# Performance work log

Hardware: AMD Instinct MI355X
Metric: run time of the kernel (lower is better)

Reference implementation:

```python
import jax, jax.numpy as jnp
import numpy as np

H, D_NOPE, D_ROPE, D_V, L_KV, HID = 16, 128, 64, 128, 512, 2048
D_QK = D_NOPE + D_ROPE
THETA = 10000.0
EPS = 1e-6


def _rope(x, positions):
    # neox-style rotary over last dim (D_ROPE); x: [T, ..., D_ROPE]
    half = D_ROPE // 2
    inv_freq = 1.0 / (THETA ** (jnp.arange(half, dtype=jnp.float32) * 2.0 / D_ROPE))
    ang = positions.astype(jnp.float32)[:, None] * inv_freq[None, :]  # [T, half]
    shape = (x.shape[0],) + (1,) * (x.ndim - 2) + (half,)
    cos, sin = jnp.cos(ang).reshape(shape), jnp.sin(ang).reshape(shape)
    x1, x2 = x[..., :half], x[..., half:]
    return jnp.concatenate([x1 * cos - x2 * sin, x2 * cos + x1 * sin], axis=-1)


def _rmsnorm(x, w):
    var = jnp.mean(x * x, axis=-1, keepdims=True)
    return x * jax.lax.rsqrt(var + EPS) * w


def setup_inputs() -> dict:
    key = jax.random.key(0)
    ks = jax.random.split(key, 6)
    T = 4096
    s = lambda fan_in: 1.0 / np.sqrt(fan_in)
    return {
        "positions": jnp.arange(T, dtype=jnp.int32),
        "hidden_states": jax.random.normal(ks[0], (T, HID), jnp.float32),
        "Wq": jax.random.normal(ks[1], (HID, H * D_QK), jnp.float32) * s(HID),
        "Wkva": jax.random.normal(ks[2], (HID, L_KV + D_ROPE), jnp.float32) * s(HID),
        "kv_a_ln_w": jnp.ones((L_KV,), jnp.float32),
        "Wkvb": jax.random.normal(ks[3], (L_KV, H * (D_NOPE + D_V)), jnp.float32) * s(L_KV),
        "Wo": jax.random.normal(ks[4], (H * D_V, HID), jnp.float32) * s(H * D_V),
    }


def reference(positions, hidden_states, Wq, Wkva, kv_a_ln_w, Wkvb, Wo):
    T = hidden_states.shape[0]
    scaling = 1.0 / np.sqrt(D_QK)

    q = (hidden_states @ Wq).reshape(T, H, D_QK)
    q_nope, q_pe = q[..., :D_NOPE], q[..., D_NOPE:]

    latent = hidden_states @ Wkva                    # [T, L_KV + D_ROPE]
    kv_a = _rmsnorm(latent[:, :L_KV], kv_a_ln_w)     # [T, L_KV]
    k_pe = latent[:, L_KV:]                          # [T, D_ROPE] (shared across heads)

    kv = (kv_a @ Wkvb).reshape(T, H, D_NOPE + D_V)
    k_nope, v = kv[..., :D_NOPE], kv[..., D_NOPE:]

    q_pe = _rope(q_pe, positions)                    # [T, H, D_ROPE]
    k_pe = _rope(k_pe, positions)                    # [T, D_ROPE]

    q = jnp.concatenate([q_nope, q_pe], axis=-1)     # [T, H, D_QK]
    k = jnp.concatenate(
        [k_nope, jnp.broadcast_to(k_pe[:, None, :], (T, H, D_ROPE))], axis=-1)

    scores = jnp.einsum("thd,shd->hts", q, k) * scaling        # [H, T, T]
    causal = positions[:, None] >= positions[None, :]           # [T, T]
    scores = jnp.where(causal[None], scores, jnp.finfo(scores.dtype).min)
    attn = jax.nn.softmax(scores, axis=-1)
    out = jnp.einsum("hts,shd->thd", attn, v)                   # [T, H, D_V]
    return out.reshape(T, H * D_V) @ Wo                          # [T, HID]
```

## Files before the change

### kernel.cpp

```cpp
#include <hip/hip_runtime.h>
#include <hip/hip_bf16.h>

#define T_LEN 4096
#define HID_DIM 2048
#define NH 16
#define DNOPE 128
#define DROPE 64
#define DV 128
#define LKV 512
#define DQK 192

#define BN 64

typedef __attribute__((ext_vector_type(8))) __bf16 bf16x8;
typedef __attribute__((ext_vector_type(4))) float f32x4;
typedef __attribute__((ext_vector_type(4))) short s16x4;

__device__ __forceinline__ unsigned short f2b(float f) {
  unsigned u = __builtin_bit_cast(unsigned, f);
  unsigned r = (u + 0x7FFFu + ((u >> 16) & 1u)) >> 16;
  return (unsigned short)r;
}

#define GL2LDS16(gp, lp)                                                   \
// ... 139 lines not shown
            float sn, cs;
            __sincosf(p * inv, &sn, &cs);
            float x1 = acc[i][j][r] * scale, x2 = acc[i][j + 2][r] * scale;
            Qb[(size_t)t * DQK + DNOPE + idx]      = f2b(x1 * cs - x2 * sn);
            Qb[(size_t)t * DQK + DNOPE + 32 + idx] = f2b(x2 * cs + x1 * sn);
          }
        }
    }
  } else {
#pragma unroll
    for (int i = 0; i < 4; i++)
#pragma unroll
      for (int j = 0; j < 4; j++) {
        int col = n0 + wn + j * 16 + l16;
        if (col < LKV + DROPE)
#pragma unroll
          for (int r = 0; r < 4; r++)
            latentf[(size_t)(row0 + i * 16 + r) * (LKV + DROPE) + col] = acc[i][j][r];
      }
  }
}

__global__ __launch_bounds__(256) void k_gemm_wkvb(
    const unsigned short* __restrict__ A, const unsigned short* __restrict__ Bt,
    unsigned short* __restrict__ Kh, unsigned short* __restrict__ VT) {
  int m0 = blockIdx.y * 128, n0 = blockIdx.x * 128;
  GEMM_CORE(A, Bt, NH * 256, LKV, LKV, LKV)
#pragma unroll
  for (int i = 0; i < 4; i++)
#pragma unroll
    for (int j = 0; j < 4; j++) {
      int col = n0 + wn + j * 16 + l16;
      int h = col >> 8, c = col & 255;
#pragma unroll
      for (int r = 0; r < 4; r++) {
        int t = row0 + i * 16 + r;
        unsigned short v = f2b(acc[i][j][r]);
        if (c < 128) Kh[((size_t)h * T_LEN + t) * DQK + c] = v;
        else         VT[((size_t)(h * 128 + c - 128)) * T_LEN + t] = v;
      }
    }
}

__global__ __launch_bounds__(256) void k_prep_latent(
    const float* __restrict__ latent, const float* __restrict__ w,
    const int* __restrict__ pos,
    unsigned short* __restrict__ kva, unsigned short* __restrict__ Kh) {
  __shared__ float red[256];
  int t = blockIdx.x;
  const float* row = latent + (size_t)t * (LKV + DROPE);
  float ss = 0.f;
  for (int c = threadIdx.x; c < LKV; c += 256) { float v = row[c]; ss += v * v; }
  red[threadIdx.x] = ss;
  __syncthreads();
  for (int s = 128; s > 0; s >>= 1) {
    if (threadIdx.x < s) red[threadIdx.x] += red[threadIdx.x + s];
    __syncthreads();
  }
  float rs = rsqrtf(red[0] / (float)LKV + 1e-6f);
  for (int c = threadIdx.x; c < LKV; c += 256)
    kva[(size_t)t * LKV + c] = f2b(row[c] * rs * w[c]);
  if (threadIdx.x < DROPE) {
    int i = threadIdx.x;
    float p = (float)pos[t];
    float val;
    if (i < 32) {
      float x1 = row[LKV + i], x2 = row[LKV + i + 32];
      float inv = __expf(-(float)i * 0.2878231366242557f);
      float sn, cs; __sincosf(p * inv, &sn, &cs);
      val = x1 * cs - x2 * sn;
    } else {
      float x1 = row[LKV + i - 32], x2 = row[LKV + i];
      float inv = __expf(-(float)(i - 32) * 0.2878231366242557f);
      float sn, cs; __sincosf(p * inv, &sn, &cs);
      val = x2 * cs + x1 * sn;
    }
    unsigned short vb = f2b(val);
#pragma unroll
    for (int h = 0; h < NH; h++)
      Kh[((size_t)h * T_LEN + t) * DQK + DNOPE + i] = vb;
  }
}

__global__ __launch_bounds__(256, 4) void k_flash(
    const unsigned short* __restrict__ Qh, const unsigned short* __restrict__ Kh,
    const unsigned short* __restrict__ VT, unsigned short* __restrict__ attn) {
  int bx = blockIdx.x;
  int h = bx & 15;
  int idx = bx >> 4;
  int qb = (idx < 32) ? (63 - idx) : (idx - 32);
  int m0 = qb * 64;
  int ntiles = qb + 1;

  __shared__ unsigned short Ks[64 * 24 * 8];
  __shared__ unsigned short Vs[128 * 8 * 8];

  int tid = threadIdx.x, lane = tid & 63, w = tid >> 6;
  int quad = lane >> 4, l16 = lane & 15;
  int x = l16 & 7;

  const unsigned short* Qbase = Qh + (size_t)h * T_LEN * DQK;
  const unsigned short* Kbase = Kh + (size_t)h * T_LEN * DQK;
  const unsigned short* Vbase = VT + (size_t)h * DV * T_LEN;

  bf16x8 qf[6];
#pragma unroll
  for (int kk = 0; kk < 6; kk++)
    qf[kk] = *(const bf16x8*)(Qbase + (size_t)(m0 + w * 16 + l16) * DQK + kk * 32 + quad * 8);

  int koff[6], voff[4];
#pragma unroll
  for (int k = 0; k < 6; k++) {
    int c = tid + k * 256;
    int row = c / 24, sc = c - row * 24;
    int cg = (sc & 0x18) | ((sc ^ row) & 7);
    koff[k] = row * DQK + cg * 8;
  }
#pragma unroll
  for (int k = 0; k < 4; k++) {
    int c = tid + k * 256;
    int row = c >> 3, sc = c & 7;
    int cg = sc ^ (row & 7);
    voff[k] = row * T_LEN + cg * 8;
  }

  const unsigned short* kEp[4];
  const unsigned short* kOp[4];
  const unsigned short* vAp[4];
#pragma unroll
  for (int st = 0; st < 4; st++) {
    int rb = (st * 16 + l16) * 192;
    kEp[st] = Ks + rb + ((quad ^ x) * 8);
    kOp[st] = Ks + rb + ((((quad + 4) ^ x)) * 8);
    vAp[st] = Vs + l16 * 64 + (((st * 2 + (quad >> 1)) ^ x) * 8) + (quad & 1) * 4;
  }

  f32x4 Oacc[8] = {};
  float li = 0.f;

#if !HAVE_MFMA16
  int lA = l16 + ((quad & 1) << 5);
  int lB = lA + 16;
  bool lowq = (quad < 2);
  const unsigned short* vFp[2];
#pragma unroll
  for (int u = 0; u < 2; u++)
    vFp[u] = Vs + l16 * 64 + (((u * 4 + quad) ^ x) * 8);
#endif

  for (int j = 0; j < ntiles; j++) {
#pragma unroll
    for (int k = 0; k < 6; k++) GL2LDS16(Kbase + koff[k], &Ks[(tid + k * 256) * 8]);
#pragma unroll
    for (int k = 0; k < 4; k++) GL2LDS16(Vbase + voff[k], &Vs[(tid + k * 256) * 8]);
#pragma unroll
    for (int k = 0; k < 6; k++) koff[k] += BN * DQK;
#pragma unroll
    for (int k = 0; k < 4; k++) voff[k] += BN;
    __syncthreads();

    f32x4 Sc[4] = {};
#pragma unroll
    for (int kk = 0; kk < 6; kk++) {
#pragma unroll
      for (int st = 0; st < 4; st++) {
        const unsigned short* kp = ((kk & 1) ? kOp[st] : kEp[st]) + (kk >> 1) * 64;
        bf16x8 kb = *(const bf16x8*)kp;
        Sc[st] = __builtin_amdgcn_mfma_f32_16x16x32_bf16(kb, qf[kk], Sc[st], 0, 0, 0);
      }
    }

    if (j == qb) {
      int m = m0 + w * 16 + l16;
      int n0 = j * BN;
#pragma unroll
      for (int st = 0; st < 4; st++)
#pragma unroll
        for (int r = 0; r < 4; r++) {
          int s = n0 + st * 16 + quad * 4 + r;
          if (s > m) Sc[st][r] = -1e30f;
        }
    }

    unsigned p0[4], p1[4];
#pragma unroll
    for (int st = 0; st < 4; st++) {
      float e0 = __expf(Sc[st][0]);
      float e1 = __expf(Sc[st][1]);
      float e2 = __expf(Sc[st][2]);
      float e3 = __expf(Sc[st][3]);
      li += (e0 + e1) + (e2 + e3);
      p0[st] = __builtin_amdgcn_perm(__builtin_bit_cast(unsigned, e1),
                                     __builtin_bit_cast(unsigned, e0), 0x07060302u);
      p1[st] = __builtin_amdgcn_perm(__builtin_bit_cast(unsigned, e3),
                                     __builtin_bit_cast(unsigned, e2), 0x07060302u);
    }

#if HAVE_MFMA16
#pragma unroll
    for (int st = 0; st < 4; st++) {
      uint2 pbu; pbu.x = p0[st]; pbu.y = p1[st];
      s16x4 pb = __builtin_bit_cast(s16x4, pbu);
#pragma unroll
      for (int dt = 0; dt < 8; dt++) {
        s16x4 va = __builtin_bit_cast(s16x4, *(const uint2*)(vAp[st] + dt * 1024));
        Oacc[dt] = mfma16(va, pb, Oacc[dt]);
      }
    }
#else
#pragma unroll
    for (int u = 0; u < 2; u++) {
      int a0 = __shfl((int)p0[2 * u], lA, 64);
      int a1 = __shfl((int)p0[2 * u + 1], lA, 64);
      int b0 = __shfl((int)p1[2 * u], lA, 64);
      int b1 = __shfl((int)p1[2 * u + 1], lA, 64);
      int c0 = __shfl((int)p0[2 * u], lB, 64);
      int c1 = __shfl((int)p0[2 * u + 1], lB, 64);
      int d0 = __shfl((int)p1[2 * u], lB, 64);
      int d1 = __shfl((int)p1[2 * u + 1], lB, 64);
      int4 pk;
      pk.x = lowq ? a0 : a1;
      pk.y = lowq ? b0 : b1;
      pk.z = lowq ? c0 : c1;
      pk.w = lowq ? d0 : d1;
      bf16x8 pb = __builtin_bit_cast(bf16x8, pk);
#pragma unroll
      for (int dt = 0; dt < 8; dt++) {
        bf16x8 va = *(const bf16x8*)(vFp[u] + dt * 1024);
        Oacc[dt] = __builtin_amdgcn_mfma_f32_16x16x32_bf16(va, pb, Oacc[dt], 0, 0, 0);
      }
    }
#endif
    __syncthreads();
  }

  li += __shfl_xor(li, 16, 64);
  li += __shfl_xor(li, 32, 64);

  float inv = 1.f / li;
  int t = m0 + w * 16 + l16;
  unsigned short* dst = attn + (size_t)t * HID_DIM + h * DV + quad * 4;
#pragma unroll
  for (int dt = 0; dt < 8; dt++) {
    unsigned lo = (unsigned)f2b(Oacc[dt][0] * inv) |
                  ((unsigned)f2b(Oacc[dt][1] * inv) << 16);
    unsigned hi = (unsigned)f2b(Oacc[dt][2] * inv) |
                  ((unsigned)f2b(Oacc[dt][3] * inv) << 16);
    uint2 pk = {lo, hi};
    *(uint2*)(dst + dt * 16) = pk;
  }
}

extern "C" void kernel_launch(void* const* d_in, const int* in_sizes, int n_in,
                              void* d_out, int out_size, void* d_ws, size_t ws_size,
                              hipStream_t stream) {
  const int*   positions = (const int*)d_in[0];
  const float* hs   = (const float*)d_in[1];
  const float* Wq   = (const float*)d_in[2];
  const float* Wkva = (const float*)d_in[3];
  const float* lnw  = (const float*)d_in[4];
  const float* Wkvb = (const float*)d_in[5];
  const float* Wo   = (const float*)d_in[6];
  float* out = (float*)d_out;

  char* p = (char*)d_ws;
  size_t off = 0;
  auto alloc = [&](size_t bytes) {
    char* r = p + off;
    off = (off + bytes + 255) & ~(size_t)255;
    return r;
  };
  unsigned short* hsb     = (unsigned short*)alloc((size_t)T_LEN * HID_DIM * 2);
  unsigned short* WqT     = (unsigned short*)alloc((size_t)(NH * DQK) * HID_DIM * 2);
  unsigned short* WkvaT   = (unsigned short*)alloc((size_t)(LKV + DROPE) * HID_DIM * 2);
  unsigned short* WkvbT   = (unsigned short*)alloc((size_t)(NH * 256) * LKV * 2);
  unsigned short* WoT     = (unsigned short*)alloc((size_t)HID_DIM * HID_DIM * 2);
  unsigned short* Qh      = (unsigned short*)alloc((size_t)NH * T_LEN * DQK * 2);
  unsigned short* kva     = (unsigned short*)alloc((size_t)T_LEN * LKV * 2);
  unsigned short* Kh      = (unsigned short*)alloc((size_t)NH * T_LEN * DQK * 2);
  unsigned short* VT      = (unsigned short*)alloc((size_t)NH * DV * T_LEN * 2);
  unsigned short* attn    = (unsigned short*)alloc((size_t)T_LEN * HID_DIM * 2);
  float*          latentf = (float*)alloc((size_t)T_LEN * (LKV + DROPE) * 4);

  k_cvt<<<(T_LEN * HID_DIM + 255) / 256, 256, 0, stream>>>(hs, hsb, T_LEN * HID_DIM);
  k_transpose_all<<<13440, dim3(32, 8), 0, stream>>>(Wq, Wkva, Wkvb, Wo, WqT, WkvaT, WkvbT, WoT);

  k_gemm_proj<<<dim3(29, T_LEN / 128), 256, 0, stream>>>(hsb, WqT, WkvaT, positions, Qh, latentf);

  k_prep_latent<<<T_LEN, 256, 0, stream>>>(latentf, lnw, positions, kva, Kh);

  k_gemm_wkvb<<<dim3((NH * 256) / 128, T_LEN / 128), 256, 0, stream>>>(kva, WkvbT, Kh, VT);

  k_flash<<<dim3(1024), 256, 0, stream>>>(Qh, Kh, VT, attn);

  k_gemm128<<<dim3(HID_DIM / 128, T_LEN / 128), 256, 0, stream>>>(
      attn, WoT, out, HID_DIM, HID_DIM, HID_DIM, HID_DIM, HID_DIM);
}
```

Before: 502.8 us.

## Pair short and long query blocks per flash block with double-buffered K/V tiles

Each flash attention workgroup now handles two query blocks, a short one (pk) and its mirror long one (63-pk). Every staged K/V tile is shared by both, which halves K/V global-to-LDS traffic for the shared prefix and balances causal work across blocks. It also double-buffers K/V in LDS so the next tile loads while the current one computes. In exchange the grid shrinks to 512 blocks, register pressure roughly doubles (occupancy hint drops from 4 to 2) and LDS per block doubles.

```diff
diff --git a/kernel.cpp b/kernel.cpp
--- a/kernel.cpp
+++ b/kernel.cpp
@@ -245,18 +245,18 @@
   }
 }
 
-__global__ __launch_bounds__(256, 4) void k_flash(
+__global__ __launch_bounds__(256, 2) void k_flash(
     const unsigned short* __restrict__ Qh, const unsigned short* __restrict__ Kh,
     const unsigned short* __restrict__ VT, unsigned short* __restrict__ attn) {
   int bx = blockIdx.x;
   int h = bx & 15;
-  int idx = bx >> 4;
-  int qb = (idx < 32) ? (63 - idx) : (idx - 32);
-  int m0 = qb * 64;
-  int ntiles = qb + 1;
-
-  __shared__ unsigned short Ks[64 * 24 * 8];
-  __shared__ unsigned short Vs[128 * 8 * 8];
+  int pk = bx >> 4;
+  int qbS = pk, qbL = 63 - pk;
+  int m0S = qbS * 64, m0L = qbL * 64;
+  int NT = qbL + 1;
+
+  __shared__ unsigned short Ks[2 * 64 * 24 * 8];
+  __shared__ unsigned short Vs[2 * 128 * 8 * 8];
 
   int tid = threadIdx.x, lane = tid & 63, w = tid >> 6;
   int quad = lane >> 4, l16 = lane & 15;
@@ -266,10 +266,12 @@
   const unsigned short* Kbase = Kh + (size_t)h * T_LEN * DQK;
   const unsigned short* Vbase = VT + (size_t)h * DV * T_LEN;
 
-  bf16x8 qf[6];
-#pragma unroll
-  for (int kk = 0; kk < 6; kk++)
-    qf[kk] = *(const bf16x8*)(Qbase + (size_t)(m0 + w * 16 + l16) * DQK + kk * 32 + quad * 8);
+  bf16x8 qfL[6], qfS[6];
+#pragma unroll
+  for (int kk = 0; kk < 6; kk++) {
+    qfL[kk] = *(const bf16x8*)(Qbase + (size_t)(m0L + w * 16 + l16) * DQK + kk * 32 + quad * 8);
+    qfS[kk] = *(const bf16x8*)(Qbase + (size_t)(m0S + w * 16 + l16) * DQK + kk * 32 + quad * 8);
+  }
 
   int koff[6], voff[4];
 #pragma unroll
@@ -287,131 +289,198 @@
     voff[k] = row * T_LEN + cg * 8;
   }
 
-  const unsigned short* kEp[4];
-  const unsigned short* kOp[4];
-  const unsigned short* vAp[4];
+  int kEo[4], kOo[4], vAo[4];
 #pragma unroll
   for (int st = 0; st < 4; st++) {
     int rb = (st * 16 + l16) * 192;
-    kEp[st] = Ks + rb + ((quad ^ x) * 8);
-    kOp[st] = Ks + rb + ((((quad + 4) ^ x)) * 8);
-    vAp[st] = Vs + l16 * 64 + (((st * 2 + (quad >> 1)) ^ x) * 8) + (quad & 1) * 4;
-  }
-
-  f32x4 Oacc[8] = {};
-  float li = 0.f;
+    kEo[st] = rb + ((quad ^ x) * 8);
+    kOo[st] = rb + (((quad + 4) ^ x) * 8);
+    vAo[st] = l16 * 64 + (((st * 2 + (quad >> 1)) ^ x) * 8) + (quad & 1) * 4;
+  }
+
+  f32x4 OaccL[8] = {}, OaccS[8] = {};
+  float liL = 0.f, liS = 0.f;
+  int mL = m0L + w * 16 + l16;
+  int mS = m0S + w * 16 + l16;
 
 #if !HAVE_MFMA16
   int lA = l16 + ((quad & 1) << 5);
   int lB = lA + 16;
   bool lowq = (quad < 2);
-  const unsigned short* vFp[2];
+  int vFo[2];
 #pragma unroll
   for (int u = 0; u < 2; u++)
-    vFp[u] = Vs + l16 * 64 + (((u * 4 + quad) ^ x) * 8);
+    vFo[u] = l16 * 64 + (((u * 4 + quad) ^ x) * 8);
 #endif
 
-  for (int j = 0; j < ntiles; j++) {
-#pragma unroll
-    for (int k = 0; k < 6; k++) GL2LDS16(Kbase + koff[k], &Ks[(tid + k * 256) * 8]);
-#pragma unroll
-    for (int k = 0; k < 4; k++) GL2LDS16(Vbase + voff[k], &Vs[(tid + k * 256) * 8]);
-#pragma unroll
-    for (int k = 0; k < 6; k++) koff[k] += BN * DQK;
-#pragma unroll
-    for (int k = 0; k < 4; k++) voff[k] += BN;
+#define STAGE(buf)                                                                         \
+  do {                                                                                     \
+    unsigned short* ksd = Ks + (buf) * (64 * 24 * 8);                                      \
+    unsigned short* vsd = Vs + (buf) * (128 * 8 * 8);                                      \
+    _Pragma("unroll")                                                                      \
+    for (int k = 0; k < 6; k++) GL2LDS16(Kbase + koff[k], &ksd[(tid + k * 256) * 8]);      \
+    _Pragma("unroll")                                                                      \
+    for (int k = 0; k < 4; k++) GL2LDS16(Vbase + voff[k], &vsd[(tid + k * 256) * 8]);      \
+    _Pragma("unroll")                                                                      \
+    for (int k = 0; k < 6; k++) koff[k] += BN * DQK;                                       \
+    _Pragma("unroll")                                                                      \
+    for (int k = 0; k < 4; k++) voff[k] += BN;                                             \
+  } while (0)
+
+#if HAVE_MFMA16
+#define TILE_PV(DOSQ)                                                                      \
+    _Pragma("unroll")                                                                      \
+    for (int st = 0; st < 4; st++) {                                                       \
+      uint2 puL; puL.x = p0L[st]; puL.y = p1L[st];                                         \
+      s16x4 pbL = __builtin_bit_cast(s16x4, puL);                                          \
+      uint2 puS; puS.x = p0S[st]; puS.y = p1S[st];                                         \
+      s16x4 pbS = __builtin_bit_cast(s16x4, puS);                                          \
+      _Pragma("unroll")                                                                    \
+      for (int dt = 0; dt < 8; dt++) {                                                     \
+        s16x4 va = __builtin_bit_cast(s16x4, *(const uint2*)(VsB + vAo[st] + dt * 1024));  \
+        OaccL[dt] = mfma16(va, pbL, OaccL[dt]);                                            \
+        if (DOSQ) OaccS[dt] = mfma16(va, pbS, OaccS[dt]);                                  \
+      }                                                                                    \
+    }
+#else
+#define TILE_PV(DOSQ)                                                                      \
+    _Pragma("unroll")                                                                      \
+    for (int u = 0; u < 2; u++) {                                                          \
+      int a0 = __shfl((int)p0L[2 * u], lA, 64);                                            \
+      int a1 = __shfl((int)p0L[2 * u + 1], lA, 64);                                        \
+      int b0 = __shfl((int)p1L[2 * u], lA, 64);                                            \
+      int b1 = __shfl((int)p1L[2 * u + 1], lA, 64);                                        \
+      int c0 = __shfl((int)p0L[2 * u], lB, 64);                                            \
+      int c1 = __shfl((int)p0L[2 * u + 1], lB, 64);                                        \
+      int d0 = __shfl((int)p1L[2 * u], lB, 64);                                            \
+      int d1 = __shfl((int)p1L[2 * u + 1], lB, 64);                                        \
+      int4 pkLv;                                                                           \
+      pkLv.x = lowq ? a0 : a1; pkLv.y = lowq ? b0 : b1;                                    \
+      pkLv.z = lowq ? c0 : c1; pkLv.w = lowq ? d0 : d1;                                    \
+      bf16x8 pbL = __builtin_bit_cast(bf16x8, pkLv);                                       \
+      int4 pkSv = pkLv;                                                                    \
+      if (DOSQ) {                                                                          \
+        int sa0 = __shfl((int)p0S[2 * u], lA, 64);                                         \
+        int sa1 = __shfl((int)p0S[2 * u + 1], lA, 64);                                     \
+        int sb0 = __shfl((int)p1S[2 * u], lA, 64);                                         \
+        int sb1 = __shfl((int)p1S[2 * u + 1], lA, 64);                                     \
+        int sc0 = __shfl((int)p0S[2 * u], lB, 64);                                         \
+        int sc1 = __shfl((int)p0S[2 * u + 1], lB, 64);                                     \
+        int sd0 = __shfl((int)p1S[2 * u], lB, 64);                                         \
+        int sd1 = __shfl((int)p1S[2 * u + 1], lB, 64);                                     \
+        pkSv.x = lowq ? sa0 : sa1; pkSv.y = lowq ? sb0 : sb1;                              \
+        pkSv.z = lowq ? sc0 : sc1; pkSv.w = lowq ? sd0 : sd1;                              \
+      }                                                                                    \
+      bf16x8 pbS = __builtin_bit_cast(bf16x8, pkSv);                                       \
+      _Pragma("unroll")                                                                    \
+      for (int dt = 0; dt < 8; dt++) {                                                     \
+        bf16x8 va = *(const bf16x8*)(VsB + vFo[u] + dt * 1024);                            \
+        OaccL[dt] = __builtin_amdgcn_mfma_f32_16x16x32_bf16(va, pbL, OaccL[dt], 0, 0, 0);  \
+        if (DOSQ) OaccS[dt] = __builtin_amdgcn_mfma_f32_16x16x32_bf16(va, pbS, OaccS[dt], 0, 0, 0); \
+      }                                                                                    \
+    }
+#endif
+
+#define TILE_BODY(DOSQ)                                                                    \
+  {                                                                                        \
+    f32x4 ScL[4] = {}; f32x4 ScS[4] = {};                                                  \
+    _Pragma("unroll")                                                                      \
+    for (int kk = 0; kk < 6; kk++) {                                                       \
+      _Pragma("unroll")                                                                    \
+      for (int st = 0; st < 4; st++) {                                                     \
+        bf16x8 kb = *(const bf16x8*)(KsB + ((kk & 1) ? kOo[st] : kEo[st]) + (kk >> 1) * 64); \
+        ScL[st] = __builtin_amdgcn_mfma_f32_16x16x32_bf16(kb, qfL[kk], ScL[st], 0, 0, 0);  \
+        if (DOSQ) ScS[st] = __builtin_amdgcn_mfma_f32_16x16x32_bf16(kb, qfS[kk], ScS[st], 0, 0, 0); \
+      }                                                                                    \
+    }                                                                                      \
+    if (j == qbL) {                                                                        \
+      _Pragma("unroll")                                                                    \
+      for (int st = 0; st < 4; st++)                                                       \
+        _Pragma("unroll")                                                                  \
+        for (int r = 0; r < 4; r++) {                                                      \
+          int s = n0 + st * 16 + quad * 4 + r;                                             \
+          if (s > mL) ScL[st][r] = -1e30f;                                                 \
+        }                                                                                  \
+    }                                                                                      \
+    if (DOSQ && j == qbS) {                                                                \
+      _Pragma("unroll")                                                                    \
+      for (int st = 0; st < 4; st++)                                                       \
+        _Pragma("unroll")                                                                  \
+        for (int r = 0; r < 4; r++) {                                                      \
+          int s = n0 + st * 16 + quad * 4 + r;                                             \
+          if (s > mS) ScS[st][r] = -1e30f;                                                 \
+        }                                                                                  \
+    }                                                                                      \
+    unsigned p0L[4], p1L[4], p0S[4], p1S[4];                                               \
+    _Pragma("unroll")                                                                      \
+    for (int st = 0; st < 4; st++) {                                                       \
+      float e0 = __expf(ScL[st][0]);                                                       \
+      float e1 = __expf(ScL[st][1]);                                                       \
+      float e2 = __expf(ScL[st][2]);                                                       \
+      float e3 = __expf(ScL[st][3]);                                                       \
+      liL += (e0 + e1) + (e2 + e3);                                                        \
+      p0L[st] = __builtin_amdgcn_perm(__builtin_bit_cast(unsigned, e1),                    \
+                                      __builtin_bit_cast(unsigned, e0), 0x07060302u);      \
+      p1L[st] = __builtin_amdgcn_perm(__builtin_bit_cast(unsigned, e3),                    \
+                                      __builtin_bit_cast(unsigned, e2), 0x07060302u);      \
+      if (DOSQ) {                                                                          \
+        float f0 = __expf(ScS[st][0]);                                                     \
+        float f1 = __expf(ScS[st][1]);                                                     \
+        float f2 = __expf(ScS[st][2]);                                                     \
+        float f3 = __expf(ScS[st][3]);                                                     \
+        liS += (f0 + f1) + (f2 + f3);                                                      \
+        p0S[st] = __builtin_amdgcn_perm(__builtin_bit_cast(unsigned, f1),                  \
+                                        __builtin_bit_cast(unsigned, f0), 0x07060302u);    \
+        p1S[st] = __builtin_amdgcn_perm(__builtin_bit_cast(unsigned, f3),                  \
+                                        __builtin_bit_cast(unsigned, f2), 0x07060302u);    \
+      } else { p0S[st] = 0; p1S[st] = 0; }                                                 \
+    }                                                                                      \
+    TILE_PV(DOSQ)                                                                          \
+  }
+
+  STAGE(0);
+  __syncthreads();
+
+  for (int j = 0; j < NT; ++j) {
+    if (j + 1 < NT) STAGE((j + 1) & 1);
+    const unsigned short* KsB = Ks + (j & 1) * (64 * 24 * 8);
+    const unsigned short* VsB = Vs + (j & 1) * (128 * 8 * 8);
+    int n0 = j * BN;
+    if (j <= pk) {
+      TILE_BODY(1)
+    } else {
+      TILE_BODY(0)
+    }
     __syncthreads();
-
-    f32x4 Sc[4] = {};
-#pragma unroll
-    for (int kk = 0; kk < 6; kk++) {
-#pragma unroll
-      for (int st = 0; st < 4; st++) {
-        const unsigned short* kp = ((kk & 1) ? kOp[st] : kEp[st]) + (kk >> 1) * 64;
-        bf16x8 kb = *(const bf16x8*)kp;
-        Sc[st] = __builtin_amdgcn_mfma_f32_16x16x32_bf16(kb, qf[kk], Sc[st], 0, 0, 0);
-      }
-    }
-
-    if (j == qb) {
-      int m = m0 + w * 16 + l16;
-      int n0 = j * BN;
-#pragma unroll
-      for (int st = 0; st < 4; st++)
-#pragma unroll
-        for (int r = 0; r < 4; r++) {
-          int s = n0 + st * 16 + quad * 4 + r;
-          if (s > m) Sc[st][r] = -1e30f;
-        }
-    }
-
-    unsigned p0[4], p1[4];
-#pragma unroll
-    for (int st = 0; st < 4; st++) {
-      float e0 = __expf(Sc[st][0]);
-      float e1 = __expf(Sc[st][1]);
-      float e2 = __expf(Sc[st][2]);
-      float e3 = __expf(Sc[st][3]);
-      li += (e0 + e1) + (e2 + e3);
-      p0[st] = __builtin_amdgcn_perm(__builtin_bit_cast(unsigned, e1),
-                                     __builtin_bit_cast(unsigned, e0), 0x07060302u);
-      p1[st] = __builtin_amdgcn_perm(__builtin_bit_cast(unsigned, e3),
-                                     __builtin_bit_cast(unsigned, e2), 0x07060302u);
-    }
-
-#if HAVE_MFMA16
-#pragma unroll
-    for (int st = 0; st < 4; st++) {
-      uint2 pbu; pbu.x = p0[st]; pbu.y = p1[st];
-      s16x4 pb = __builtin_bit_cast(s16x4, pbu);
-#pragma unroll
-      for (int dt = 0; dt < 8; dt++) {
-        s16x4 va = __builtin_bit_cast(s16x4, *(const uint2*)(vAp[st] + dt * 1024));
-        Oacc[dt] = mfma16(va, pb, Oacc[dt]);
-      }
-    }
-#else
-#pragma unroll
-    for (int u = 0; u < 2; u++) {
-      int a0 = __shfl((int)p0[2 * u], lA, 64);
-      int a1 = __shfl((int)p0[2 * u + 1], lA, 64);
-      int b0 = __shfl((int)p1[2 * u], lA, 64);
-      int b1 = __shfl((int)p1[2 * u + 1], lA, 64);
-      int c0 = __shfl((int)p0[2 * u], lB, 64);
-      int c1 = __shfl((int)p0[2 * u + 1], lB, 64);
-      int d0 = __shfl((int)p1[2 * u], lB, 64);
-      int d1 = __shfl((int)p1[2 * u + 1], lB, 64);
-      int4 pk;
-      pk.x = lowq ? a0 : a1;
-      pk.y = lowq ? b0 : b1;
-      pk.z = lowq ? c0 : c1;
-      pk.w = lowq ? d0 : d1;
-      bf16x8 pb = __builtin_bit_cast(bf16x8, pk);
-#pragma unroll
-      for (int dt = 0; dt < 8; dt++) {
-        bf16x8 va = *(const bf16x8*)(vFp[u] + dt * 1024);
-        Oacc[dt] = __builtin_amdgcn_mfma_f32_16x16x32_bf16(va, pb, Oacc[dt], 0, 0, 0);
-      }
-    }
-#endif
-    __syncthreads();
-  }
-
-  li += __shfl_xor(li, 16, 64);
-  li += __shfl_xor(li, 32, 64);
-
-  float inv = 1.f / li;
-  int t = m0 + w * 16 + l16;
-  unsigned short* dst = attn + (size_t)t * HID_DIM + h * DV + quad * 4;
+  }
+
+  liL += __shfl_xor(liL, 16, 64);
+  liL += __shfl_xor(liL, 32, 64);
+  liS += __shfl_xor(liS, 16, 64);
+  liS += __shfl_xor(liS, 32, 64);
+
+  float invL = 1.f / liL;
+  float invS = 1.f / liS;
+  unsigned short* dstL = attn + (size_t)mL * HID_DIM + h * DV + quad * 4;
+  unsigned short* dstS = attn + (size_t)mS * HID_DIM + h * DV + quad * 4;
 #pragma unroll
   for (int dt = 0; dt < 8; dt++) {
-    unsigned lo = (unsigned)f2b(Oacc[dt][0] * inv) |
-                  ((unsigned)f2b(Oacc[dt][1] * inv) << 16);
-    unsigned hi = (unsigned)f2b(Oacc[dt][2] * inv) |
-                  ((unsigned)f2b(Oacc[dt][3] * inv) << 16);
-    uint2 pk = {lo, hi};
-    *(uint2*)(dst + dt * 16) = pk;
-  }
+    unsigned lo = (unsigned)f2b(OaccL[dt][0] * invL) |
+                  ((unsigned)f2b(OaccL[dt][1] * invL) << 16);
+    unsigned hi = (unsigned)f2b(OaccL[dt][2] * invL) |
+                  ((unsigned)f2b(OaccL[dt][3] * invL) << 16);
+    uint2 pkv = {lo, hi};
+    *(uint2*)(dstL + dt * 16) = pkv;
+    unsigned lo2 = (unsigned)f2b(OaccS[dt][0] * invS) |
+                   ((unsigned)f2b(OaccS[dt][1] * invS) << 16);
+    unsigned hi2 = (unsigned)f2b(OaccS[dt][2] * invS) |
+                   ((unsigned)f2b(OaccS[dt][3] * invS) << 16);
+    uint2 pkv2 = {lo2, hi2};
+    *(uint2*)(dstS + dt * 16) = pkv2;
+  }
+#undef STAGE
+#undef TILE_PV
+#undef TILE_BODY
 }
 
 extern "C" void kernel_launch(void* const* d_in, const int* in_sizes, int n_in,
@@ -454,7 +523,7 @@
 
   k_gemm_wkvb<<<dim3((NH * 256) / 128, T_LEN / 128), 256, 0, stream>>>(kva, WkvbT, Kh, VT);
 
-  k_flash<<<dim3(1024), 256, 0, stream>>>(Qh, Kh, VT, attn);
+  k_flash<<<dim3(512), 256, 0, stream>>>(Qh, Kh, VT, attn);
 
   k_gemm128<<<dim3(HID_DIM / 128, T_LEN / 128), 256, 0, stream>>>(
       attn, WoT, out, HID_DIM, HID_DIM, HID_DIM, HID_DIM, HID_DIM);
```

Result: no change. 502.7 us (-0.0%).

## Process two query sub-blocks per flash block and split long rows across blocks

Applied to the files above, without the earlier changes.

The flash kernel now handles a 128-row query block as two 64-row halves that share each loaded K/V tile, doubling MFMA work per LDS load. For the 16 longest query blocks per head, the KV range is split between two workgroups that write fp32 partial outputs and row sums. A new merge kernel adds the partials and normalizes them. The Opart buffer reuses workspace whose contents are dead by then, and workspace allocations are reordered to allow this. The change costs extra registers (occupancy hint lowered from 4 to 3), an extra kernel launch, and fp32 partial traffic.

```diff
diff --git a/kernel.cpp b/kernel.cpp
--- a/kernel.cpp
+++ b/kernel.cpp
@@ -245,15 +245,26 @@
   }
 }
 
-__global__ __launch_bounds__(256, 4) void k_flash(
+__global__ __launch_bounds__(256, 3) void k_flash(
     const unsigned short* __restrict__ Qh, const unsigned short* __restrict__ Kh,
-    const unsigned short* __restrict__ VT, unsigned short* __restrict__ attn) {
+    const unsigned short* __restrict__ VT, unsigned short* __restrict__ attn,
+    float* __restrict__ Opart, float* __restrict__ Oli) {
   int bx = blockIdx.x;
-  int h = bx & 15;
-  int idx = bx >> 4;
-  int qb = (idx < 32) ? (63 - idx) : (idx - 32);
-  int m0 = qb * 64;
-  int ntiles = qb + 1;
+  int slot = bx >> 8;
+  int r = bx & 255;
+  int h = r & 15;
+  int tt = r >> 4;
+  int qb, ch, j0, j1;
+  bool split;
+  if (slot < 2) {
+    qb = 16 + tt; ch = slot; split = true;
+    if (ch == 0) { j0 = 0;      j1 = qb; }
+    else         { j0 = qb + 1; j1 = 2 * qb + 1; }
+  } else {
+    qb = 15 - tt; ch = 0; split = false; j0 = 0; j1 = 2 * qb + 1;
+  }
+  int m0 = qb * 128;
+  int diagA = 2 * qb, diagB = 2 * qb + 1;
 
   __shared__ unsigned short Ks[64 * 24 * 8];
   __shared__ unsigned short Vs[128 * 8 * 8];
@@ -266,10 +277,12 @@
   const unsigned short* Kbase = Kh + (size_t)h * T_LEN * DQK;
   const unsigned short* Vbase = VT + (size_t)h * DV * T_LEN;
 
-  bf16x8 qf[6];
-#pragma unroll
-  for (int kk = 0; kk < 6; kk++)
-    qf[kk] = *(const bf16x8*)(Qbase + (size_t)(m0 + w * 16 + l16) * DQK + kk * 32 + quad * 8);
+  bf16x8 qfS[6], qfL[6];
+#pragma unroll
+  for (int kk = 0; kk < 6; kk++) {
+    qfS[kk] = *(const bf16x8*)(Qbase + (size_t)(m0 + w * 16 + l16) * DQK + kk * 32 + quad * 8);
+    qfL[kk] = *(const bf16x8*)(Qbase + (size_t)(m0 + 64 + w * 16 + l16) * DQK + kk * 32 + quad * 8);
+  }
 
   int koff[6], voff[4];
 #pragma unroll
@@ -277,41 +290,41 @@
     int c = tid + k * 256;
     int row = c / 24, sc = c - row * 24;
     int cg = (sc & 0x18) | ((sc ^ row) & 7);
-    koff[k] = row * DQK + cg * 8;
+    koff[k] = row * DQK + cg * 8 + j0 * BN * DQK;
   }
 #pragma unroll
   for (int k = 0; k < 4; k++) {
     int c = tid + k * 256;
     int row = c >> 3, sc = c & 7;
     int cg = sc ^ (row & 7);
-    voff[k] = row * T_LEN + cg * 8;
-  }
-
-  const unsigned short* kEp[4];
-  const unsigned short* kOp[4];
-  const unsigned short* vAp[4];
+    voff[k] = row * T_LEN + cg * 8 + j0 * BN;
+  }
+
+  int kEo[4], kOo[4], vAo[4];
 #pragma unroll
   for (int st = 0; st < 4; st++) {
     int rb = (st * 16 + l16) * 192;
-    kEp[st] = Ks + rb + ((quad ^ x) * 8);
-    kOp[st] = Ks + rb + ((((quad + 4) ^ x)) * 8);
-    vAp[st] = Vs + l16 * 64 + (((st * 2 + (quad >> 1)) ^ x) * 8) + (quad & 1) * 4;
-  }
-
-  f32x4 Oacc[8] = {};
-  float li = 0.f;
+    kEo[st] = rb + ((quad ^ x) * 8);
+    kOo[st] = rb + (((quad + 4) ^ x) * 8);
+    vAo[st] = l16 * 64 + (((st * 2 + (quad >> 1)) ^ x) * 8) + (quad & 1) * 4;
+  }
+
+  f32x4 OaccS[8] = {}, OaccL[8] = {};
+  float liS = 0.f, liL = 0.f;
+  int mS = m0 + w * 16 + l16;
+  int mL = mS + 64;
 
 #if !HAVE_MFMA16
   int lA = l16 + ((quad & 1) << 5);
   int lB = lA + 16;
   bool lowq = (quad < 2);
-  const unsigned short* vFp[2];
+  int vFo[2];
 #pragma unroll
   for (int u = 0; u < 2; u++)
-    vFp[u] = Vs + l16 * 64 + (((u * 4 + quad) ^ x) * 8);
+    vFo[u] = l16 * 64 + (((u * 4 + quad) ^ x) * 8);
 #endif
 
-  for (int j = 0; j < ntiles; j++) {
+  for (int j = j0; j <= j1; ++j) {
 #pragma unroll
     for (int k = 0; k < 6; k++) GL2LDS16(Kbase + koff[k], &Ks[(tid + k * 256) * 8]);
 #pragma unroll
@@ -322,95 +335,174 @@
     for (int k = 0; k < 4; k++) voff[k] += BN;
     __syncthreads();
 
-    f32x4 Sc[4] = {};
+    f32x4 ScS[4] = {}, ScL[4] = {};
 #pragma unroll
     for (int kk = 0; kk < 6; kk++) {
 #pragma unroll
       for (int st = 0; st < 4; st++) {
-        const unsigned short* kp = ((kk & 1) ? kOp[st] : kEp[st]) + (kk >> 1) * 64;
-        bf16x8 kb = *(const bf16x8*)kp;
-        Sc[st] = __builtin_amdgcn_mfma_f32_16x16x32_bf16(kb, qf[kk], Sc[st], 0, 0, 0);
+        bf16x8 kb = *(const bf16x8*)(Ks + ((kk & 1) ? kOo[st] : kEo[st]) + (kk >> 1) * 64);
+        ScS[st] = __builtin_amdgcn_mfma_f32_16x16x32_bf16(kb, qfS[kk], ScS[st], 0, 0, 0);
+        ScL[st] = __builtin_amdgcn_mfma_f32_16x16x32_bf16(kb, qfL[kk], ScL[st], 0, 0, 0);
       }
     }
 
-    if (j == qb) {
-      int m = m0 + w * 16 + l16;
-      int n0 = j * BN;
+    int n0 = j * BN;
+    if (j >= diagA) {
 #pragma unroll
       for (int st = 0; st < 4; st++)
 #pragma unroll
         for (int r = 0; r < 4; r++) {
           int s = n0 + st * 16 + quad * 4 + r;
-          if (s > m) Sc[st][r] = -1e30f;
+          if (s > mS) ScS[st][r] = -1e30f;
         }
     }
-
-    unsigned p0[4], p1[4];
+    if (j == diagB) {
+#pragma unroll
+      for (int st = 0; st < 4; st++)
+#pragma unroll
+        for (int r = 0; r < 4; r++) {
+          int s = n0 + st * 16 + quad * 4 + r;
+          if (s > mL) ScL[st][r] = -1e30f;
+        }
+    }
+
+    unsigned p0S[4], p1S[4], p0L[4], p1L[4];
 #pragma unroll
     for (int st = 0; st < 4; st++) {
-      float e0 = __expf(Sc[st][0]);
-      float e1 = __expf(Sc[st][1]);
-      float e2 = __expf(Sc[st][2]);
-      float e3 = __expf(Sc[st][3]);
-      li += (e0 + e1) + (e2 + e3);
-      p0[st] = __builtin_amdgcn_perm(__builtin_bit_cast(unsigned, e1),
-                                     __builtin_bit_cast(unsigned, e0), 0x07060302u);
-      p1[st] = __builtin_amdgcn_perm(__builtin_bit_cast(unsigned, e3),
-                                     __builtin_bit_cast(unsigned, e2), 0x07060302u);
+      float e0 = __expf(ScS[st][0]);
+      float e1 = __expf(ScS[st][1]);
+      float e2 = __expf(ScS[st][2]);
+      float e3 = __expf(ScS[st][3]);
+      liS += (e0 + e1) + (e2 + e3);
+      p0S[st] = __builtin_amdgcn_perm(__builtin_bit_cast(unsigned, e1),
+                                      __builtin_bit_cast(unsigned, e0), 0x07060302u);
+      p1S[st] = __builtin_amdgcn_perm(__builtin_bit_cast(unsigned, e3),
+                                      __builtin_bit_cast(unsigned, e2), 0x07060302u);
+      float f0 = __expf(ScL[st][0]);
+      float f1 = __expf(ScL[st][1]);
+      float f2 = __expf(ScL[st][2]);
+      float f3 = __expf(ScL[st][3]);
+      liL += (f0 + f1) + (f2 + f3);
+      p0L[st] = __builtin_amdgcn_perm(__builtin_bit_cast(unsigned, f1),
+                                      __builtin_bit_cast(unsigned, f0), 0x07060302u);
+      p1L[st] = __builtin_amdgcn_perm(__builtin_bit_cast(unsigned, f3),
+                                      __builtin_bit_cast(unsigned, f2), 0x07060302u);
     }
 
 #if HAVE_MFMA16
 #pragma unroll
     for (int st = 0; st < 4; st++) {
-      uint2 pbu; pbu.x = p0[st]; pbu.y = p1[st];
-      s16x4 pb = __builtin_bit_cast(s16x4, pbu);
+      uint2 puS; puS.x = p0S[st]; puS.y = p1S[st];
+      s16x4 pbS = __builtin_bit_cast(s16x4, puS);
+      uint2 puL; puL.x = p0L[st]; puL.y = p1L[st];
+      s16x4 pbL = __builtin_bit_cast(s16x4, puL);
 #pragma unroll
       for (int dt = 0; dt < 8; dt++) {
-        s16x4 va = __builtin_bit_cast(s16x4, *(const uint2*)(vAp[st] + dt * 1024));
-        Oacc[dt] = mfma16(va, pb, Oacc[dt]);
+        s16x4 va = __builtin_bit_cast(s16x4, *(const uint2*)(Vs + vAo[st] + dt * 1024));
+        OaccS[dt] = mfma16(va, pbS, OaccS[dt]);
+        OaccL[dt] = mfma16(va, pbL, OaccL[dt]);
       }
     }
 #else
 #pragma unroll
     for (int u = 0; u < 2; u++) {
-      int a0 = __shfl((int)p0[2 * u], lA, 64);
-      int a1 = __shfl((int)p0[2 * u + 1], lA, 64);
-      int b0 = __shfl((int)p1[2 * u], lA, 64);
-      int b1 = __shfl((int)p1[2 * u + 1], lA, 64);
-      int c0 = __shfl((int)p0[2 * u], lB, 64);
-      int c1 = __shfl((int)p0[2 * u + 1], lB, 64);
-      int d0 = __shfl((int)p1[2 * u], lB, 64);
-      int d1 = __shfl((int)p1[2 * u + 1], lB, 64);
-      int4 pk;
-      pk.x = lowq ? a0 : a1;
-      pk.y = lowq ? b0 : b1;
-      pk.z = lowq ? c0 : c1;
-      pk.w = lowq ? d0 : d1;
-      bf16x8 pb = __builtin_bit_cast(bf16x8, pk);
+      int a0 = __shfl((int)p0S[2 * u], lA, 64);
+      int a1 = __shfl((int)p0S[2 * u + 1], lA, 64);
+      int b0 = __shfl((int)p1S[2 * u], lA, 64);
+      int b1 = __shfl((int)p1S[2 * u + 1], lA, 64);
+      int c0 = __shfl((int)p0S[2 * u], lB, 64);
+      int c1 = __shfl((int)p0S[2 * u + 1], lB, 64);
+      int d0 = __shfl((int)p1S[2 * u], lB, 64);
+      int d1 = __shfl((int)p1S[2 * u + 1], lB, 64);
+      int4 pkS;
+      pkS.x = lowq ? a0 : a1; pkS.y = lowq ? b0 : b1;
+      pkS.z = lowq ? c0 : c1; pkS.w = lowq ? d0 : d1;
+      bf16x8 pbS = __builtin_bit_cast(bf16x8, pkS);
+      int sa0 = __shfl((int)p0L[2 * u], lA, 64);
+      int sa1 = __shfl((int)p0L[2 * u + 1], lA, 64);
+      int sb0 = __shfl((int)p1L[2 * u], lA, 64);
+      int sb1 = __shfl((int)p1L[2 * u + 1], lA, 64);
+      int sc0 = __shfl((int)p0L[2 * u], lB, 64);
+      int sc1 = __shfl((int)p0L[2 * u + 1], lB, 64);
+      int sd0 = __shfl((int)p1L[2 * u], lB, 64);
+      int sd1 = __shfl((int)p1L[2 * u + 1], lB, 64);
+      int4 pkL;
+      pkL.x = lowq ? sa0 : sa1; pkL.y = lowq ? sb0 : sb1;
+      pkL.z = lowq ? sc0 : sc1; pkL.w = lowq ? sd0 : sd1;
+      bf16x8 pbL = __builtin_bit_cast(bf16x8, pkL);
 #pragma unroll
       for (int dt = 0; dt < 8; dt++) {
-        bf16x8 va = *(const bf16x8*)(vFp[u] + dt * 1024);
-        Oacc[dt] = __builtin_amdgcn_mfma_f32_16x16x32_bf16(va, pb, Oacc[dt], 0, 0, 0);
+        bf16x8 va = *(const bf16x8*)(Vs + vFo[u] + dt * 1024);
+        OaccS[dt] = __builtin_amdgcn_mfma_f32_16x16x32_bf16(va, pbS, OaccS[dt], 0, 0, 0);
+        OaccL[dt] = __builtin_amdgcn_mfma_f32_16x16x32_bf16(va, pbL, OaccL[dt], 0, 0, 0);
       }
     }
 #endif
     __syncthreads();
   }
 
-  li += __shfl_xor(li, 16, 64);
-  li += __shfl_xor(li, 32, 64);
-
-  float inv = 1.f / li;
-  int t = m0 + w * 16 + l16;
-  unsigned short* dst = attn + (size_t)t * HID_DIM + h * DV + quad * 4;
-#pragma unroll
-  for (int dt = 0; dt < 8; dt++) {
-    unsigned lo = (unsigned)f2b(Oacc[dt][0] * inv) |
-                  ((unsigned)f2b(Oacc[dt][1] * inv) << 16);
-    unsigned hi = (unsigned)f2b(Oacc[dt][2] * inv) |
-                  ((unsigned)f2b(Oacc[dt][3] * inv) << 16);
-    uint2 pk = {lo, hi};
-    *(uint2*)(dst + dt * 16) = pk;
+  liS += __shfl_xor(liS, 16, 64);
+  liS += __shfl_xor(liS, 32, 64);
+  liL += __shfl_xor(liL, 16, 64);
+  liL += __shfl_xor(liL, 32, 64);
+
+  if (!split) {
+    float invS = 1.f / liS;
+    float invL = 1.f / liL;
+    unsigned short* dstS = attn + (size_t)mS * HID_DIM + h * DV + quad * 4;
+    unsigned short* dstL = attn + (size_t)mL * HID_DIM + h * DV + quad * 4;
+#pragma unroll
+    for (int dt = 0; dt < 8; dt++) {
+      unsigned lo = (unsigned)f2b(OaccS[dt][0] * invS) |
+                    ((unsigned)f2b(OaccS[dt][1] * invS) << 16);
+      unsigned hi = (unsigned)f2b(OaccS[dt][2] * invS) |
+                    ((unsigned)f2b(OaccS[dt][3] * invS) << 16);
+      uint2 pkv = {lo, hi};
+      *(uint2*)(dstS + dt * 16) = pkv;
+      unsigned lo2 = (unsigned)f2b(OaccL[dt][0] * invL) |
+                     ((unsigned)f2b(OaccL[dt][1] * invL) << 16);
+      unsigned hi2 = (unsigned)f2b(OaccL[dt][2] * invL) |
+                     ((unsigned)f2b(OaccL[dt][3] * invL) << 16);
+      uint2 pkv2 = {lo2, hi2};
+      *(uint2*)(dstL + dt * 16) = pkv2;
+    }
+  } else {
+    int pidx = ((h << 4) | (qb - 16)) * 2 + ch;
+    float* Ob = Opart + (size_t)pidx * (128 * 128);
+    float* Lb = Oli + (size_t)pidx * 128;
+    int rA = w * 16 + l16;
+#pragma unroll
+    for (int dt = 0; dt < 8; dt++) {
+      *(f32x4*)&Ob[(size_t)rA * 128 + dt * 16 + quad * 4] = OaccS[dt];
+      *(f32x4*)&Ob[(size_t)(rA + 64) * 128 + dt * 16 + quad * 4] = OaccL[dt];
+    }
+    if (quad == 0) { Lb[rA] = liS; Lb[rA + 64] = liL; }
+  }
+}
+
+__global__ __launch_bounds__(256) void k_merge(const float* __restrict__ Opart,
+                                               const float* __restrict__ Oli,
+                                               unsigned short* __restrict__ attn) {
+  int pidx = blockIdx.x;
+  int h = pidx >> 4, qb = 16 + (pidx & 15);
+  const float* O0 = Opart + (size_t)(pidx * 2 + 0) * (128 * 128);
+  const float* O1 = Opart + (size_t)(pidx * 2 + 1) * (128 * 128);
+  const float* L0 = Oli + (size_t)(pidx * 2 + 0) * 128;
+  const float* L1 = Oli + (size_t)(pidx * 2 + 1) * 128;
+  int tid = threadIdx.x;
+  int row = tid >> 1, c0 = (tid & 1) * 64;
+  float inv = 1.f / (L0[row] + L1[row]);
+  unsigned short* dst = attn + (size_t)(qb * 128 + row) * HID_DIM + h * DV + c0;
+#pragma unroll 4
+  for (int cc = 0; cc < 64; cc += 4) {
+    f32x4 a = *(const f32x4*)&O0[(size_t)row * 128 + c0 + cc];
+    f32x4 b = *(const f32x4*)&O1[(size_t)row * 128 + c0 + cc];
+    unsigned lo = (unsigned)f2b((a[0] + b[0]) * inv) |
+                  ((unsigned)f2b((a[1] + b[1]) * inv) << 16);
+    unsigned hi = (unsigned)f2b((a[2] + b[2]) * inv) |
+                  ((unsigned)f2b((a[3] + b[3]) * inv) << 16);
+    uint2 pkv = {lo, hi};
+    *(uint2*)(dst + cc) = pkv;
   }
 }
 
@@ -433,17 +525,22 @@
     off = (off + bytes + 255) & ~(size_t)255;
     return r;
   };
+  unsigned short* WoT     = (unsigned short*)alloc((size_t)HID_DIM * HID_DIM * 2);
+  unsigned short* Qh      = (unsigned short*)alloc((size_t)NH * T_LEN * DQK * 2);
+  unsigned short* Kh      = (unsigned short*)alloc((size_t)NH * T_LEN * DQK * 2);
+  unsigned short* VT      = (unsigned short*)alloc((size_t)NH * DV * T_LEN * 2);
+  unsigned short* attn    = (unsigned short*)alloc((size_t)T_LEN * HID_DIM * 2);
+  size_t poolbase = off;
   unsigned short* hsb     = (unsigned short*)alloc((size_t)T_LEN * HID_DIM * 2);
   unsigned short* WqT     = (unsigned short*)alloc((size_t)(NH * DQK) * HID_DIM * 2);
   unsigned short* WkvaT   = (unsigned short*)alloc((size_t)(LKV + DROPE) * HID_DIM * 2);
   unsigned short* WkvbT   = (unsigned short*)alloc((size_t)(NH * 256) * LKV * 2);
-  unsigned short* WoT     = (unsigned short*)alloc((size_t)HID_DIM * HID_DIM * 2);
-  unsigned short* Qh      = (unsigned short*)alloc((size_t)NH * T_LEN * DQK * 2);
   unsigned short* kva     = (unsigned short*)alloc((size_t)T_LEN * LKV * 2);
-  unsigned short* Kh      = (unsigned short*)alloc((size_t)NH * T_LEN * DQK * 2);
-  unsigned short* VT      = (unsigned short*)alloc((size_t)NH * DV * T_LEN * 2);
-  unsigned short* attn    = (unsigned short*)alloc((size_t)T_LEN * HID_DIM * 2);
   float*          latentf = (float*)alloc((size_t)T_LEN * (LKV + DROPE) * 4);
+  size_t opart_bytes = (size_t)512 * 128 * 128 * 4;
+  float* Opart = (float*)(p + poolbase);
+  size_t oli_off = poolbase + ((opart_bytes + 255) & ~(size_t)255);
+  float* Oli = (float*)(p + oli_off);
 
   k_cvt<<<(T_LEN * HID_DIM + 255) / 256, 256, 0, stream>>>(hs, hsb, T_LEN * HID_DIM);
   k_transpose_all<<<13440, dim3(32, 8), 0, stream>>>(Wq, Wkva, Wkvb, Wo, WqT, WkvaT, WkvbT, WoT);
@@ -454,7 +551,8 @@
 
   k_gemm_wkvb<<<dim3((NH * 256) / 128, T_LEN / 128), 256, 0, stream>>>(kva, WkvbT, Kh, VT);
 
-  k_flash<<<dim3(1024), 256, 0, stream>>>(Qh, Kh, VT, attn);
+  k_flash<<<dim3(768), 256, 0, stream>>>(Qh, Kh, VT, attn, Opart, Oli);
+  k_merge<<<dim3(256), 256, 0, stream>>>(Opart, Oli, attn);
 
   k_gemm128<<<dim3(HID_DIM / 128, T_LEN / 128), 256, 0, stream>>>(
       attn, WoT, out, HID_DIM, HID_DIM, HID_DIM, HID_DIM, HID_DIM);
```

After: 588.0 us. 16.9% more time.

## Use 128-row query tiles with 512-thread blocks in flash attention

Applied to the files above, without the earlier changes.

The flash kernel now has each block handle 128 query rows with 8 waves instead of 64 rows with 4 waves, so each K/V tile loaded into LDS is shared by twice as many query rows. This halves the global-to-LDS traffic per query row. The diagonal tiles are handled per wave: the first four waves skip the last tile and each half masks its own diagonal. The cost is fewer blocks (512), lower occupancy per CU, and some idle waves on the final diagonal tile.

```diff
diff --git a/kernel.cpp b/kernel.cpp
--- a/kernel.cpp
+++ b/kernel.cpp
@@ -245,15 +245,16 @@
   }
 }
 
-__global__ __launch_bounds__(256, 4) void k_flash(
+__global__ __launch_bounds__(512, 2) void k_flash(
     const unsigned short* __restrict__ Qh, const unsigned short* __restrict__ Kh,
     const unsigned short* __restrict__ VT, unsigned short* __restrict__ attn) {
   int bx = blockIdx.x;
   int h = bx & 15;
-  int idx = bx >> 4;
-  int qb = (idx < 32) ? (63 - idx) : (idx - 32);
-  int m0 = qb * 64;
-  int ntiles = qb + 1;
+  int t = (bx & 255) >> 4;
+  int qb = (bx < 256) ? (31 - t) : t;
+  int m0 = qb * 128;
+  int diagA = 2 * qb, diagB = 2 * qb + 1;
+  int NT = 2 * qb + 2;
 
   __shared__ unsigned short Ks[64 * 24 * 8];
   __shared__ unsigned short Vs[128 * 8 * 8];
@@ -271,129 +272,129 @@
   for (int kk = 0; kk < 6; kk++)
     qf[kk] = *(const bf16x8*)(Qbase + (size_t)(m0 + w * 16 + l16) * DQK + kk * 32 + quad * 8);
 
-  int koff[6], voff[4];
-#pragma unroll
-  for (int k = 0; k < 6; k++) {
-    int c = tid + k * 256;
+  int koff[3], voff[2];
+#pragma unroll
+  for (int k = 0; k < 3; k++) {
+    int c = tid + k * 512;
     int row = c / 24, sc = c - row * 24;
     int cg = (sc & 0x18) | ((sc ^ row) & 7);
     koff[k] = row * DQK + cg * 8;
   }
 #pragma unroll
-  for (int k = 0; k < 4; k++) {
-    int c = tid + k * 256;
+  for (int k = 0; k < 2; k++) {
+    int c = tid + k * 512;
     int row = c >> 3, sc = c & 7;
     int cg = sc ^ (row & 7);
     voff[k] = row * T_LEN + cg * 8;
   }
 
-  const unsigned short* kEp[4];
-  const unsigned short* kOp[4];
-  const unsigned short* vAp[4];
+  int kEo[4], kOo[4], vAo[4];
 #pragma unroll
   for (int st = 0; st < 4; st++) {
     int rb = (st * 16 + l16) * 192;
-    kEp[st] = Ks + rb + ((quad ^ x) * 8);
-    kOp[st] = Ks + rb + ((((quad + 4) ^ x)) * 8);
-    vAp[st] = Vs + l16 * 64 + (((st * 2 + (quad >> 1)) ^ x) * 8) + (quad & 1) * 4;
+    kEo[st] = rb + ((quad ^ x) * 8);
+    kOo[st] = rb + (((quad + 4) ^ x) * 8);
+    vAo[st] = l16 * 64 + (((st * 2 + (quad >> 1)) ^ x) * 8) + (quad & 1) * 4;
   }
 
   f32x4 Oacc[8] = {};
   float li = 0.f;
+  int m = m0 + w * 16 + l16;
+  int dj = (w < 4) ? diagA : diagB;
 
 #if !HAVE_MFMA16
   int lA = l16 + ((quad & 1) << 5);
   int lB = lA + 16;
   bool lowq = (quad < 2);
-  const unsigned short* vFp[2];
+  int vFo[2];
 #pragma unroll
   for (int u = 0; u < 2; u++)
-    vFp[u] = Vs + l16 * 64 + (((u * 4 + quad) ^ x) * 8);
+    vFo[u] = l16 * 64 + (((u * 4 + quad) ^ x) * 8);
 #endif
 
-  for (int j = 0; j < ntiles; j++) {
-#pragma unroll
-    for (int k = 0; k < 6; k++) GL2LDS16(Kbase + koff[k], &Ks[(tid + k * 256) * 8]);
-#pragma unroll
-    for (int k = 0; k < 4; k++) GL2LDS16(Vbase + voff[k], &Vs[(tid + k * 256) * 8]);
-#pragma unroll
-    for (int k = 0; k < 6; k++) koff[k] += BN * DQK;
-#pragma unroll
-    for (int k = 0; k < 4; k++) voff[k] += BN;
+  for (int j = 0; j < NT; ++j) {
+#pragma unroll
+    for (int k = 0; k < 3; k++) GL2LDS16(Kbase + koff[k], &Ks[(tid + k * 512) * 8]);
+#pragma unroll
+    for (int k = 0; k < 2; k++) GL2LDS16(Vbase + voff[k], &Vs[(tid + k * 512) * 8]);
+#pragma unroll
+    for (int k = 0; k < 3; k++) koff[k] += BN * DQK;
+#pragma unroll
+    for (int k = 0; k < 2; k++) voff[k] += BN;
     __syncthreads();
 
-    f32x4 Sc[4] = {};
-#pragma unroll
-    for (int kk = 0; kk < 6; kk++) {
+    if (!(j == diagB && w < 4)) {
+      f32x4 Sc[4] = {};
+#pragma unroll
+      for (int kk = 0; kk < 6; kk++) {
+#pragma unroll
+        for (int st = 0; st < 4; st++) {
+          bf16x8 kb = *(const bf16x8*)(Ks + ((kk & 1) ? kOo[st] : kEo[st]) + (kk >> 1) * 64);
+          Sc[st] = __builtin_amdgcn_mfma_f32_16x16x32_bf16(kb, qf[kk], Sc[st], 0, 0, 0);
+        }
+      }
+
+      if (j == dj) {
+        int n0 = j * BN;
+#pragma unroll
+        for (int st = 0; st < 4; st++)
+#pragma unroll
+          for (int r = 0; r < 4; r++) {
+            int s = n0 + st * 16 + quad * 4 + r;
+            if (s > m) Sc[st][r] = -1e30f;
+          }
+      }
+
+      unsigned p0[4], p1[4];
 #pragma unroll
       for (int st = 0; st < 4; st++) {
-        const unsigned short* kp = ((kk & 1) ? kOp[st] : kEp[st]) + (kk >> 1) * 64;
-        bf16x8 kb = *(const bf16x8*)kp;
-        Sc[st] = __builtin_amdgcn_mfma_f32_16x16x32_bf16(kb, qf[kk], Sc[st], 0, 0, 0);
-      }
+        float e0 = __expf(Sc[st][0]);
+        float e1 = __expf(Sc[st][1]);
+        float e2 = __expf(Sc[st][2]);
+        float e3 = __expf(Sc[st][3]);
+        li += (e0 + e1) + (e2 + e3);
+        p0[st] = __builtin_amdgcn_perm(__builtin_bit_cast(unsigned, e1),
+                                       __builtin_bit_cast(unsigned, e0), 0x07060302u);
+        p1[st] = __builtin_amdgcn_perm(__builtin_bit_cast(unsigned, e3),
+                                       __builtin_bit_cast(unsigned, e2), 0x07060302u);
+      }
+
+#if HAVE_MFMA16
+#pragma unroll
+      for (int st = 0; st < 4; st++) {
+        uint2 pbu; pbu.x = p0[st]; pbu.y = p1[st];
+        s16x4 pb = __builtin_bit_cast(s16x4, pbu);
+#pragma unroll
+        for (int dt = 0; dt < 8; dt++) {
+          s16x4 va = __builtin_bit_cast(s16x4, *(const uint2*)(Vs + vAo[st] + dt * 1024));
+          Oacc[dt] = mfma16(va, pb, Oacc[dt]);
+        }
+      }
+#else
+#pragma unroll
+      for (int u = 0; u < 2; u++) {
+        int a0 = __shfl((int)p0[2 * u], lA, 64);
+        int a1 = __shfl((int)p0[2 * u + 1], lA, 64);
+        int b0 = __shfl((int)p1[2 * u], lA, 64);
+        int b1 = __shfl((int)p1[2 * u + 1], lA, 64);
+        int c0 = __shfl((int)p0[2 * u], lB, 64);
+        int c1 = __shfl((int)p0[2 * u + 1], lB, 64);
+        int d0 = __shfl((int)p1[2 * u], lB, 64);
+        int d1 = __shfl((int)p1[2 * u + 1], lB, 64);
+        int4 pk;
+        pk.x = lowq ? a0 : a1;
+        pk.y = lowq ? b0 : b1;
+        pk.z = lowq ? c0 : c1;
+        pk.w = lowq ? d0 : d1;
+        bf16x8 pb = __builtin_bit_cast(bf16x8, pk);
+#pragma unroll
+        for (int dt = 0; dt < 8; dt++) {
+          bf16x8 va = *(const bf16x8*)(Vs + vFo[u] + dt * 1024);
+          Oacc[dt] = __builtin_amdgcn_mfma_f32_16x16x32_bf16(va, pb, Oacc[dt], 0, 0, 0);
+        }
+      }
+#endif
     }
-
-    if (j == qb) {
-      int m = m0 + w * 16 + l16;
-      int n0 = j * BN;
-#pragma unroll
-      for (int st = 0; st < 4; st++)
-#pragma unroll
-        for (int r = 0; r < 4; r++) {
-          int s = n0 + st * 16 + quad * 4 + r;
-          if (s > m) Sc[st][r] = -1e30f;
-        }
-    }
-
-    unsigned p0[4], p1[4];
-#pragma unroll
-    for (int st = 0; st < 4; st++) {
-      float e0 = __expf(Sc[st][0]);
-      float e1 = __expf(Sc[st][1]);
-      float e2 = __expf(Sc[st][2]);
-      float e3 = __expf(Sc[st][3]);
-      li += (e0 + e1) + (e2 + e3);
-      p0[st] = __builtin_amdgcn_perm(__builtin_bit_cast(unsigned, e1),
-                                     __builtin_bit_cast(unsigned, e0), 0x07060302u);
-      p1[st] = __builtin_amdgcn_perm(__builtin_bit_cast(unsigned, e3),
-                                     __builtin_bit_cast(unsigned, e2), 0x07060302u);
-    }
-
-#if HAVE_MFMA16
-#pragma unroll
-    for (int st = 0; st < 4; st++) {
-      uint2 pbu; pbu.x = p0[st]; pbu.y = p1[st];
-      s16x4 pb = __builtin_bit_cast(s16x4, pbu);
-#pragma unroll
-      for (int dt = 0; dt < 8; dt++) {
-        s16x4 va = __builtin_bit_cast(s16x4, *(const uint2*)(vAp[st] + dt * 1024));
-        Oacc[dt] = mfma16(va, pb, Oacc[dt]);
-      }
-    }
-#else
-#pragma unroll
-    for (int u = 0; u < 2; u++) {
-      int a0 = __shfl((int)p0[2 * u], lA, 64);
-      int a1 = __shfl((int)p0[2 * u + 1], lA, 64);
-      int b0 = __shfl((int)p1[2 * u], lA, 64);
-      int b1 = __shfl((int)p1[2 * u + 1], lA, 64);
-      int c0 = __shfl((int)p0[2 * u], lB, 64);
-      int c1 = __shfl((int)p0[2 * u + 1], lB, 64);
-      int d0 = __shfl((int)p1[2 * u], lB, 64);
-      int d1 = __shfl((int)p1[2 * u + 1], lB, 64);
-      int4 pk;
-      pk.x = lowq ? a0 : a1;
-      pk.y = lowq ? b0 : b1;
-      pk.z = lowq ? c0 : c1;
-      pk.w = lowq ? d0 : d1;
-      bf16x8 pb = __builtin_bit_cast(bf16x8, pk);
-#pragma unroll
-      for (int dt = 0; dt < 8; dt++) {
-        bf16x8 va = *(const bf16x8*)(vFp[u] + dt * 1024);
-        Oacc[dt] = __builtin_amdgcn_mfma_f32_16x16x32_bf16(va, pb, Oacc[dt], 0, 0, 0);
-      }
-    }
-#endif
     __syncthreads();
   }
 
@@ -401,8 +402,7 @@
   li += __shfl_xor(li, 32, 64);
 
   float inv = 1.f / li;
-  int t = m0 + w * 16 + l16;
-  unsigned short* dst = attn + (size_t)t * HID_DIM + h * DV + quad * 4;
+  unsigned short* dst = attn + (size_t)m * HID_DIM + h * DV + quad * 4;
 #pragma unroll
   for (int dt = 0; dt < 8; dt++) {
     unsigned lo = (unsigned)f2b(Oacc[dt][0] * inv) |
@@ -454,7 +454,7 @@
 
   k_gemm_wkvb<<<dim3((NH * 256) / 128, T_LEN / 128), 256, 0, stream>>>(kva, WkvbT, Kh, VT);
 
-  k_flash<<<dim3(1024), 256, 0, stream>>>(Qh, Kh, VT, attn);
+  k_flash<<<dim3(512), 512, 0, stream>>>(Qh, Kh, VT, attn);
 
   k_gemm128<<<dim3(HID_DIM / 128, T_LEN / 128), 256, 0, stream>>>(
       attn, WoT, out, HID_DIM, HID_DIM, HID_DIM, HID_DIM, HID_DIM);
```

After: 514.0 us. 1.02x slower.
